# Performance work log

Hardware: AMD Instinct MI355X
Metric: run time of the kernel (lower is better)

Reference implementation:

```python
import jax, jax.numpy as jnp
import numpy as np

N = 50000          # nodes
E = 1_600_000      # edges (avg degree 32)
G = 512            # graphs in batch
IN_DIM = 128
HID = 64


def setup_inputs() -> dict:
    key = jax.random.key(0)
    ks = jax.random.split(key, 9)
    x = jax.random.normal(ks[0], (N, IN_DIM), dtype=jnp.float32)
    edge_index = jax.random.randint(ks[1], (2, E), 0, N, dtype=jnp.int64)
    edge_attr = jax.random.uniform(ks[2], (E,), dtype=jnp.float32)
    batch = jnp.sort(jax.random.randint(ks[3], (N,), 0, G, dtype=jnp.int64))
    W1 = jax.random.normal(ks[4], (IN_DIM, HID), dtype=jnp.float32) / np.sqrt(IN_DIM)
    b1 = jnp.zeros((HID,), dtype=jnp.float32)
    W2 = jax.random.normal(ks[5], (HID, HID), dtype=jnp.float32) / np.sqrt(HID)
    b2 = jnp.zeros((HID,), dtype=jnp.float32)
    Wlin = jax.random.normal(ks[6], (HID, 1), dtype=jnp.float32) / np.sqrt(HID)
    blin = jnp.zeros((1,), dtype=jnp.float32)
    return {"x": x, "edge_index": edge_index, "edge_attr": edge_attr,
            "batch": batch, "W1": W1, "b1": b1, "W2": W2, "b2": b2,
            "Wlin": Wlin, "blin": blin}


def reference(x, edge_index, edge_attr, batch, W1, b1, W2, b2, Wlin, blin):
    n = x.shape[0]
    src, dst = edge_index[0], edge_index[1]
    # GCNConv: add self-loops with weight 1, symmetric normalization
    loop = jnp.arange(n)
    src_f = jnp.concatenate([src, loop])
    dst_f = jnp.concatenate([dst, loop])
    w = jnp.concatenate([edge_attr, jnp.ones((n,), x.dtype)])
    deg = jax.ops.segment_sum(w, dst_f, num_segments=n)
    dis = jnp.where(deg > 0, jax.lax.rsqrt(jnp.maximum(deg, 1e-12)), 0.0)
    norm = dis[src_f] * w * dis[dst_f]  # [E+N]

    def conv(h, W, b):
        hw = h @ W                          # [N, HID]
        msg = norm[:, None] * hw[src_f]     # [E+N, HID]
        return jax.ops.segment_sum(msg, dst_f, num_segments=n) + b

    h = jax.nn.relu(conv(x, W1, b1))
    h = conv(h, W2, b2)
    # global_mean_pool over graph ids
    counts = jax.ops.segment_sum(jnp.ones((n,), h.dtype), batch, num_segments=G)
    pooled = jax.ops.segment_sum(h, batch, num_segments=G) / jnp.maximum(counts, 1.0)[:, None]
    return pooled @ Wlin + blin  # [G, 1]
```

## Files before the change

### kernel.cpp

```cpp
#include <hip/hip_runtime.h>

#define NN 50000
#define NE 1600000
#define NG 512
#define IN_DIM 128
#define HID 64

#define NB 128
#define NBK ((NN + NB - 1) / NB)
#define EBLK 512
#define EPB (NE / EBLK)

typedef unsigned short ushort_t;
typedef unsigned int uint_t;

static __device__ __forceinline__ ushort_t f2bf(float f) {
    uint_t u = __float_as_uint(f);
    u += 0x7FFFu + ((u >> 16) & 1u);
    return (ushort_t)(u >> 16);
}
static __device__ __forceinline__ float bflo(uint_t u) { return __uint_as_float(u << 16); }
static __device__ __forceinline__ float bfhi(uint_t u) { return __uint_as_float(u & 0xFFFF0000u); }

__global__ void cnt_kernel(const int* __restrict__ ei, int* __restrict__ pcnt) {
    __shared__ int h[NBK];
    for (int i = threadIdx.x; i < NBK; i += blockDim.x) h[i] = 0;
    __syncthreads();
    int base = blockIdx.x * EPB;
    for (int e = base + threadIdx.x; e < base + EPB; e += blockDim.x)
        atomicAdd(&h[ei[NE + e] >> 7], 1);
    __syncthreads();
    for (int i = threadIdx.x; i < NBK; i += blockDim.x)
        pcnt[(size_t)i * EBLK + blockIdx.x] = h[i];
}

__global__ void bscan_kernel(int* __restrict__ pcnt, int* __restrict__ tot) {
    __shared__ int s[EBLK];
    int k = blockIdx.x, t = threadIdx.x;
    int v = pcnt[(size_t)k * EBLK + t];
    s[t] = v;
    __syncthreads();
    for (int off = 1; off < EBLK; off <<= 1) {
        int add = (t >= off) ? s[t - off] : 0;
        __syncthreads();
        s[t] += add;
        __syncthreads();
    }
    pcnt[(size_t)k * EBLK + t] = s[t] - v;
    if (t == EBLK - 1) tot[k] = s[t];
}

__global__ void tscan_kernel(const int* __restrict__ tot, int* __restrict__ bbase) {
    __shared__ int s[512];
    int t = threadIdx.x;
    int v = (t < NBK) ? tot[t] : 0;
    s[t] = v;
    __syncthreads();
    for (int off = 1; off < 512; off <<= 1) {
        int add = (t >= off) ? s[t - off] : 0;
        __syncthreads();
        s[t] += add;
        __syncthreads();
    }
    if (t < NBK) bbase[t] = s[t] - v;
    if (t == NBK - 1) bbase[NBK] = s[t];
}

__global__ void scatter_kernel(const int* __restrict__ ei, const float* __restrict__ ea,
                               const int* __restrict__ pcnt, const int* __restrict__ bbase,
                               int2* __restrict__ recs) {
    __shared__ int curs[NBK];
    int b = blockIdx.x;
    for (int i = threadIdx.x; i < NBK; i += blockDim.x)
        curs[i] = bbase[i] + pcnt[(size_t)i * EBLK + b];
    __syncthreads();
    int base = b * EPB;
    for (int e = base + threadIdx.x; e < base + EPB; e += blockDim.x) {
        int dst = ei[NE + e];
        int src = ei[e];
        int k = dst >> 7;
        int pos = atomicAdd(&curs[k], 1);
        recs[pos] = make_int2(((dst & 127) << 17) | src, __float_as_int(ea[e]));
    }
}

__global__ void binfo2_kernel(const int2* __restrict__ recs, const int* __restrict__ bbase,
                              int* __restrict__ indeg, float* __restrict__ dis,
                              int* __restrict__ offs, int2* __restrict__ csr) {
    __shared__ float deg[NB];
    __shared__ int cnt[NB];
    __shared__ int sc[NB];
    __shared__ int curs[NB];
    __shared__ float wdst[NB];
    int k = blockIdx.x;
    int lo = k * NB;
    int nLoc = min(NB, NN - lo);
    int tid = threadIdx.x;
    for (int i = tid; i < nLoc; i += blockDim.x) { deg[i] = 0.f; cnt[i] = 0; }
    __syncthreads();
    int start = bbase[k], end = bbase[k + 1];
    for (int e = start + tid; e < end; e += blockDim.x) {
        int2 r = recs[e];
        int dl = r.x >> 17;
        atomicAdd(&deg[dl], __int_as_float(r.y));
        atomicAdd(&cnt[dl], 1);
    }
    __syncthreads();
    for (int i = tid; i < nLoc; i += blockDim.x) {
        float d = rsqrtf(deg[i] + 1.0f);
        wdst[i] = d;
        dis[lo + i] = d;
        indeg[lo + i] = cnt[i];
    }
    if (tid < NB) sc[tid] = (tid < nLoc) ? cnt[tid] : 0;
    __syncthreads();
    for (int off = 1; off < NB; off <<= 1) {
        int add = (tid < NB && tid >= off) ? sc[tid - off] : 0;
        __syncthreads();
        if (tid < NB) sc[tid] += add;
        __syncthreads();
    }
    if (tid < nLoc) {
        int ex = start + sc[tid] - cnt[tid];
        offs[lo + tid] = ex;
        curs[tid] = ex;
    }
    __syncthreads();
    for (int e = start + tid; e < end; e += blockDim.x) {
        int2 r = recs[e];
        int src = r.x & 0x1FFFF;
        int dl = r.x >> 17;
        float pw = __int_as_float(r.y) * wdst[dl];
        int pos = atomicAdd(&curs[dl], 1);
        csr[pos] = make_int2(src, __float_as_int(pw));
    }
}

template <int K>
__global__ __launch_bounds__(256) void gemm_kernel(const float* __restrict__ X,
                                                   const float* __restrict__ W,
                                                   const float* __restrict__ dis,
                                                   ushort_t* __restrict__ Yb) {
    __shared__ float w_lds[K * HID];
    __shared__ float x_lds[K][65];
    int tid = threadIdx.x;
    int rowbase = blockIdx.x * 64;
    for (int i = tid; i < K * HID; i += 256) w_lds[i] = W[i];
    for (int i = tid; i < 16 * K; i += 256) {
        int row = i / (K / 4);
        int k4 = i % (K / 4);
        int r = rowbase + row;
        float4 v = (r < NN) ? ((const float4*)(X + (size_t)r * K))[k4]
                            : make_float4(0.f, 0.f, 0.f, 0.f);
        x_lds[k4 * 4 + 0][row] = v.x;
        x_lds[k4 * 4 + 1][row] = v.y;
        x_lds[k4 * 4 + 2][row] = v.z;
        x_lds[k4 * 4 + 3][row] = v.w;
    }
    __syncthreads();
    int c0 = (tid & 15) * 4;
    int r0 = (tid >> 4) * 4;
    float acc[4][4] = {};
#pragma unroll 4
    for (int k = 0; k < K; ++k) {
        float x0 = x_lds[k][r0 + 0];
        float x1 = x_lds[k][r0 + 1];
        float x2 = x_lds[k][r0 + 2];
        float x3 = x_lds[k][r0 + 3];
        float4 wv = *(const float4*)&w_lds[k * HID + c0];
        acc[0][0] += x0 * wv.x; acc[0][1] += x0 * wv.y; acc[0][2] += x0 * wv.z; acc[0][3] += x0 * wv.w;
        acc[1][0] += x1 * wv.x; acc[1][1] += x1 * wv.y; acc[1][2] += x1 * wv.z; acc[1][3] += x1 * wv.w;
        acc[2][0] += x2 * wv.x; acc[2][1] += x2 * wv.y; acc[2][2] += x2 * wv.z; acc[2][3] += x2 * wv.w;
        acc[3][0] += x3 * wv.x; acc[3][1] += x3 * wv.y; acc[3][2] += x3 * wv.z; acc[3][3] += x3 * wv.w;
    }
#pragma unroll
    for (int i = 0; i < 4; ++i) {
        int r = rowbase + r0 + i;
        if (r < NN) {
            float dr = dis[r];
            ushort4 o;
            o.x = f2bf(dr * acc[i][0]); o.y = f2bf(dr * acc[i][1]);
            o.z = f2bf(dr * acc[i][2]); o.w = f2bf(dr * acc[i][3]);
            *(ushort4*)&Yb[(size_t)r * HID + c0] = o;
        }
    }
}

__global__ void gather1_kernel(const int2* __restrict__ csr,
                               const int* __restrict__ offs,
                               const int* __restrict__ indeg,
                               const float* __restrict__ dis,
                               const ushort_t* __restrict__ A1,
                               const float* __restrict__ b1,
                               float* __restrict__ OUT) {
    int node = blockIdx.x * 4 + (threadIdx.x >> 6);
    int lane = threadIdx.x & 63;
    if (node >= NN) return;
    int o  = lane >> 3;
    int cl = lane & 7;
    int start = offs[node];
    int n = indeg[node];
    float a0 = 0.f, a1 = 0.f, a2 = 0.f, a3 = 0.f;
    float a4 = 0.f, a5 = 0.f, a6 = 0.f, a7 = 0.f;
    for (int c = 0; c < n; c += 64) {
        int idx = c + lane;
        int2 rec = (idx < n) ? csr[start + idx] : make_int2(0, 0);
        int tmax = min(n - c, 64);
#pragma unroll 2
        for (int t = 0; t * 8 < tmax; ++t) {
            int sl = t * 8 + o;
            int key = __shfl(rec.x, sl, 64);
            float w = __int_as_float(__shfl(rec.y, sl, 64));
            uint4 v = *(const uint4*)(A1 + ((size_t)key << 6) + (cl << 3));
            a0 += w * bflo(v.x); a1 += w * bfhi(v.x);
            a2 += w * bflo(v.y); a3 += w * bfhi(v.y);
            a4 += w * bflo(v.z); a5 += w * bfhi(v.z);
            a6 += w * bflo(v.w); a7 += w * bfhi(v.w);
        }
    }
    a0 += __shfl_xor(a0, 8, 64); a0 += __shfl_xor(a0, 16, 64); a0 += __shfl_xor(a0, 32, 64);
    a1 += __shfl_xor(a1, 8, 64); a1 += __shfl_xor(a1, 16, 64); a1 += __shfl_xor(a1, 32, 64);
    a2 += __shfl_xor(a2, 8, 64); a2 += __shfl_xor(a2, 16, 64); a2 += __shfl_xor(a2, 32, 64);
    a3 += __shfl_xor(a3, 8, 64); a3 += __shfl_xor(a3, 16, 64); a3 += __shfl_xor(a3, 32, 64);
    a4 += __shfl_xor(a4, 8, 64); a4 += __shfl_xor(a4, 16, 64); a4 += __shfl_xor(a4, 32, 64);
    a5 += __shfl_xor(a5, 8, 64); a5 += __shfl_xor(a5, 16, 64); a5 += __shfl_xor(a5, 32, 64);
    a6 += __shfl_xor(a6, 8, 64); a6 += __shfl_xor(a6, 16, 64); a6 += __shfl_xor(a6, 32, 64);
    a7 += __shfl_xor(a7, 8, 64); a7 += __shfl_xor(a7, 16, 64); a7 += __shfl_xor(a7, 32, 64);
    if (o == 0) {
        float d = dis[node];
        uint4 sv = *(const uint4*)(A1 + ((size_t)node << 6) + (cl << 3));
        const float4* bv = (const float4*)(b1 + (cl << 3));
        float4 bA = bv[0], bB = bv[1];
        float o0 = fmaxf(a0 + d * bflo(sv.x) + bA.x, 0.f);
        float o1 = fmaxf(a1 + d * bfhi(sv.x) + bA.y, 0.f);
        float o2 = fmaxf(a2 + d * bflo(sv.y) + bA.z, 0.f);
        float o3 = fmaxf(a3 + d * bfhi(sv.y) + bA.w, 0.f);
        float o4 = fmaxf(a4 + d * bflo(sv.z) + bB.x, 0.f);
        float o5 = fmaxf(a5 + d * bfhi(sv.z) + bB.y, 0.f);
        float o6 = fmaxf(a6 + d * bflo(sv.w) + bB.z, 0.f);
        float o7 = fmaxf(a7 + d * bfhi(sv.w) + bB.w, 0.f);
        float* op = &OUT[((size_t)node << 6) + (cl << 3)];
        *(float4*)op       = make_float4(o0, o1, o2, o3);
        *(float4*)(op + 4) = make_float4(o4, o5, o6, o7);
    }
}

__global__ void gather2_kernel(const int2* __restrict__ csr,
                               const int* __restrict__ offs,
                               const int* __restrict__ indeg,
                               const float* __restrict__ dis,
                               const ushort_t* __restrict__ A2,
                               const float* __restrict__ b2,
                               const float* __restrict__ Wlin,
                               float* __restrict__ nodeval) {
    int node = blockIdx.x * 4 + (threadIdx.x >> 6);
    int lane = threadIdx.x & 63;
    if (node >= NN) return;
    int o  = lane >> 3;
    int cl = lane & 7;
    int start = offs[node];
    int n = indeg[node];
    float a0 = 0.f, a1 = 0.f, a2 = 0.f, a3 = 0.f;
    float a4 = 0.f, a5 = 0.f, a6 = 0.f, a7 = 0.f;
    for (int c = 0; c < n; c += 64) {
        int idx = c + lane;
        int2 rec = (idx < n) ? csr[start + idx] : make_int2(0, 0);
        int tmax = min(n - c, 64);
#pragma unroll 2
        for (int t = 0; t * 8 < tmax; ++t) {
            int sl = t * 8 + o;
            int key = __shfl(rec.x, sl, 64);
            float w = __int_as_float(__shfl(rec.y, sl, 64));
            uint4 v = *(const uint4*)(A2 + ((size_t)key << 6) + (cl << 3));
            a0 += w * bflo(v.x); a1 += w * bfhi(v.x);
            a2 += w * bflo(v.y); a3 += w * bfhi(v.y);
            a4 += w * bflo(v.z); a5 += w * bfhi(v.z);
            a6 += w * bflo(v.w); a7 += w * bfhi(v.w);
        }
    }
    a0 += __shfl_xor(a0, 8, 64); a0 += __shfl_xor(a0, 16, 64); a0 += __shfl_xor(a0, 32, 64);
    a1 += __shfl_xor(a1, 8, 64); a1 += __shfl_xor(a1, 16, 64); a1 += __shfl_xor(a1, 32, 64);
    a2 += __shfl_xor(a2, 8, 64); a2 += __shfl_xor(a2, 16, 64); a2 += __shfl_xor(a2, 32, 64);
    a3 += __shfl_xor(a3, 8, 64); a3 += __shfl_xor(a3, 16, 64); a3 += __shfl_xor(a3, 32, 64);
    a4 += __shfl_xor(a4, 8, 64); a4 += __shfl_xor(a4, 16, 64); a4 += __shfl_xor(a4, 32, 64);
    a5 += __shfl_xor(a5, 8, 64); a5 += __shfl_xor(a5, 16, 64); a5 += __shfl_xor(a5, 32, 64);
    a6 += __shfl_xor(a6, 8, 64); a6 += __shfl_xor(a6, 16, 64); a6 += __shfl_xor(a6, 32, 64);
    a7 += __shfl_xor(a7, 8, 64); a7 += __shfl_xor(a7, 16, 64); a7 += __shfl_xor(a7, 32, 64);
    float d = dis[node];
    uint4 sv = *(const uint4*)(A2 + ((size_t)node << 6) + (cl << 3));
    const float4* bv = (const float4*)(b2 + (cl << 3));
    float4 bA = bv[0], bB = bv[1];
    const float4* wv = (const float4*)(Wlin + (cl << 3));
    float4 wA = wv[0], wB = wv[1];
    float dot = (a0 + d * bflo(sv.x) + bA.x) * wA.x
              + (a1 + d * bfhi(sv.x) + bA.y) * wA.y
              + (a2 + d * bflo(sv.y) + bA.z) * wA.z
              + (a3 + d * bfhi(sv.y) + bA.w) * wA.w
              + (a4 + d * bflo(sv.z) + bB.x) * wB.x
              + (a5 + d * bfhi(sv.z) + bB.y) * wB.y
              + (a6 + d * bflo(sv.w) + bB.z) * wB.z
              + (a7 + d * bfhi(sv.w) + bB.w) * wB.w;
    dot += __shfl_xor(dot, 1, 64);
    dot += __shfl_xor(dot, 2, 64);
    dot += __shfl_xor(dot, 4, 64);
    if (lane == 0) nodeval[node] = dot;
}

__global__ void pool_final_kernel(const float* __restrict__ nodeval,
                                  const int* __restrict__ batch,
                                  const float* __restrict__ blin,
                                  float* __restrict__ out) {
    __shared__ int bnd[2];
    __shared__ float red[4];
    int g = blockIdx.x;
    if (threadIdx.x < 2) {
        int target = g + threadIdx.x;
        int lo = 0, hi = NN;
        while (lo < hi) {
            int mid = (lo + hi) >> 1;
            if (batch[mid] < target) lo = mid + 1; else hi = mid;
        }
        bnd[threadIdx.x] = lo;
    }
    __syncthreads();
    int s = bnd[0], e = bnd[1];
    float a = 0.f;
    for (int i = s + threadIdx.x; i < e; i += 256) a += nodeval[i];
    for (int off = 32; off > 0; off >>= 1) a += __shfl_down(a, off, 64);
    int lane = threadIdx.x & 63;
    int wv = threadIdx.x >> 6;
    if (lane == 0) red[wv] = a;
    __syncthreads();
    if (threadIdx.x == 0) {
        float t = red[0] + red[1] + red[2] + red[3];
        out[g] = t / fmaxf((float)(e - s), 1.0f) + blin[0];
    }
}

extern "C" void kernel_launch(void* const* d_in, const int* in_sizes, int n_in,
                              void* d_out, int out_size, void* d_ws, size_t ws_size,
                              hipStream_t stream) {
    const float* x     = (const float*)d_in[0];
    const int*   ei    = (const int*)d_in[1];
    const float* ea    = (const float*)d_in[2];
    const int*   batch = (const int*)d_in[3];
    const float* W1    = (const float*)d_in[4];
    const float* b1    = (const float*)d_in[5];
    const float* W2    = (const float*)d_in[6];
    const float* b2    = (const float*)d_in[7];
    const float* Wlin  = (const float*)d_in[8];
    const float* blin  = (const float*)d_in[9];
    float*       out   = (float*)d_out;

    char* ws = (char*)d_ws;
    auto alloc = [&](size_t bytes) {
        void* p = (void*)ws;
        ws += (bytes + 255) / 256 * 256;
        return p;
    };
    float*    dis     = (float*)alloc((size_t)NN * 4);
    int*      indeg   = (int*)alloc((size_t)NN * 4);
    int*      offs    = (int*)alloc((size_t)NN * 4);
    int*      pcnt    = (int*)alloc((size_t)NBK * EBLK * 4);
    int*      tot     = (int*)alloc((size_t)NBK * 4);
    int*      bbase   = (int*)alloc((size_t)(NBK + 1) * 4);
    int2*     recs    = (int2*)alloc((size_t)NE * 8);
    int2*     csr     = (int2*)alloc((size_t)NE * 8);
    float*    B       = (float*)alloc((size_t)NN * HID * 4);
    float*    nodeval = (float*)alloc((size_t)NN * 4);
    ushort_t* A1      = (ushort_t*)recs;
    ushort_t* A2      = (ushort_t*)recs + (size_t)NN * HID;

    cnt_kernel<<<EBLK, 256, 0, stream>>>(ei, pcnt);
    bscan_kernel<<<NBK, EBLK, 0, stream>>>(pcnt, tot);
    tscan_kernel<<<1, 512, 0, stream>>>(tot, bbase);
    scatter_kernel<<<EBLK, 256, 0, stream>>>(ei, ea, pcnt, bbase, recs);
    binfo2_kernel<<<NBK, 256, 0, stream>>>(recs, bbase, indeg, dis, offs, csr);

    gemm_kernel<IN_DIM><<<(NN + 63) / 64, 256, 0, stream>>>(x, W1, dis, A1);
    gather1_kernel<<<(NN + 3) / 4, 256, 0, stream>>>(csr, offs, indeg, dis, A1, b1, B);

    gemm_kernel<HID><<<(NN + 63) / 64, 256, 0, stream>>>(B, W2, dis, A2);
    gather2_kernel<<<(NN + 3) / 4, 256, 0, stream>>>(csr, offs, indeg, dis, A2, b2,
                                                     Wlin, nodeval);

    pool_final_kernel<<<NG, 256, 0, stream>>>(nodeval, batch, blin, out);
}
```

Before: 162.4 us.

## Fuse graph CSR build kernels into one cooperative kernel with grid syncs

```diff
diff --git a/kernel.cpp b/kernel.cpp
--- a/kernel.cpp
+++ b/kernel.cpp
@@ -1,4 +1,7 @@
 #include <hip/hip_runtime.h>
+#include <hip/hip_cooperative_groups.h>
+
+namespace cg = cooperative_groups;
 
 #define NN 50000
 #define NE 1600000
@@ -22,117 +25,130 @@
 static __device__ __forceinline__ float bflo(uint_t u) { return __uint_as_float(u << 16); }
 static __device__ __forceinline__ float bfhi(uint_t u) { return __uint_as_float(u & 0xFFFF0000u); }
 
-__global__ void cnt_kernel(const int* __restrict__ ei, int* __restrict__ pcnt) {
+__global__ void build_kernel(const int* __restrict__ ei, const float* __restrict__ ea,
+                             int* __restrict__ pcnt, int* __restrict__ tot,
+                             int* __restrict__ bbase, int* __restrict__ indeg,
+                             float* __restrict__ dis, int* __restrict__ offs,
+                             int2* __restrict__ recs, int2* __restrict__ csr) {
+    cg::grid_group grid = cg::this_grid();
+    int b = blockIdx.x;
+    int tid = threadIdx.x;
+
     __shared__ int h[NBK];
-    for (int i = threadIdx.x; i < NBK; i += blockDim.x) h[i] = 0;
-    __syncthreads();
-    int base = blockIdx.x * EPB;
-    for (int e = base + threadIdx.x; e < base + EPB; e += blockDim.x)
-        atomicAdd(&h[ei[NE + e] >> 7], 1);
-    __syncthreads();
-    for (int i = threadIdx.x; i < NBK; i += blockDim.x)
-        pcnt[(size_t)i * EBLK + blockIdx.x] = h[i];
-}
-
-__global__ void bscan_kernel(int* __restrict__ pcnt, int* __restrict__ tot) {
-    __shared__ int s[EBLK];
-    int k = blockIdx.x, t = threadIdx.x;
-    int v = pcnt[(size_t)k * EBLK + t];
-    s[t] = v;
-    __syncthreads();
-    for (int off = 1; off < EBLK; off <<= 1) {
-        int add = (t >= off) ? s[t - off] : 0;
-        __syncthreads();
-        s[t] += add;
-        __syncthreads();
-    }
-    pcnt[(size_t)k * EBLK + t] = s[t] - v;
-    if (t == EBLK - 1) tot[k] = s[t];
-}
-
-__global__ void tscan_kernel(const int* __restrict__ tot, int* __restrict__ bbase) {
-    __shared__ int s[512];
-    int t = threadIdx.x;
-    int v = (t < NBK) ? tot[t] : 0;
-    s[t] = v;
-    __syncthreads();
-    for (int off = 1; off < 512; off <<= 1) {
-        int add = (t >= off) ? s[t - off] : 0;
-        __syncthreads();
-        s[t] += add;
-        __syncthreads();
-    }
-    if (t < NBK) bbase[t] = s[t] - v;
-    if (t == NBK - 1) bbase[NBK] = s[t];
-}
-
-__global__ void scatter_kernel(const int* __restrict__ ei, const float* __restrict__ ea,
-                               const int* __restrict__ pcnt, const int* __restrict__ bbase,
-                               int2* __restrict__ recs) {
-    __shared__ int curs[NBK];
-    int b = blockIdx.x;
-    for (int i = threadIdx.x; i < NBK; i += blockDim.x)
-        curs[i] = bbase[i] + pcnt[(size_t)i * EBLK + b];
-    __syncthreads();
-    int base = b * EPB;
-    for (int e = base + threadIdx.x; e < base + EPB; e += blockDim.x) {
-        int dst = ei[NE + e];
-        int src = ei[e];
-        int k = dst >> 7;
-        int pos = atomicAdd(&curs[k], 1);
-        recs[pos] = make_int2(((dst & 127) << 17) | src, __float_as_int(ea[e]));
-    }
-}
-
-__global__ void binfo2_kernel(const int2* __restrict__ recs, const int* __restrict__ bbase,
-                              int* __restrict__ indeg, float* __restrict__ dis,
-                              int* __restrict__ offs, int2* __restrict__ csr) {
-    __shared__ float deg[NB];
-    __shared__ int cnt[NB];
+    __shared__ int s[256];
+    __shared__ float degs[NB];
+    __shared__ int cnts[NB];
     __shared__ int sc[NB];
     __shared__ int curs[NB];
     __shared__ float wdst[NB];
-    int k = blockIdx.x;
-    int lo = k * NB;
-    int nLoc = min(NB, NN - lo);
-    int tid = threadIdx.x;
-    for (int i = tid; i < nLoc; i += blockDim.x) { deg[i] = 0.f; cnt[i] = 0; }
-    __syncthreads();
-    int start = bbase[k], end = bbase[k + 1];
-    for (int e = start + tid; e < end; e += blockDim.x) {
-        int2 r = recs[e];
-        int dl = r.x >> 17;
-        atomicAdd(&deg[dl], __int_as_float(r.y));
-        atomicAdd(&cnt[dl], 1);
-    }
-    __syncthreads();
-    for (int i = tid; i < nLoc; i += blockDim.x) {
-        float d = rsqrtf(deg[i] + 1.0f);
-        wdst[i] = d;
-        dis[lo + i] = d;
-        indeg[lo + i] = cnt[i];
-    }
-    if (tid < NB) sc[tid] = (tid < nLoc) ? cnt[tid] : 0;
-    __syncthreads();
-    for (int off = 1; off < NB; off <<= 1) {
-        int add = (tid < NB && tid >= off) ? sc[tid - off] : 0;
-        __syncthreads();
-        if (tid < NB) sc[tid] += add;
-        __syncthreads();
-    }
-    if (tid < nLoc) {
-        int ex = start + sc[tid] - cnt[tid];
-        offs[lo + tid] = ex;
-        curs[tid] = ex;
-    }
-    __syncthreads();
-    for (int e = start + tid; e < end; e += blockDim.x) {
-        int2 r = recs[e];
-        int src = r.x & 0x1FFFF;
-        int dl = r.x >> 17;
-        float pw = __int_as_float(r.y) * wdst[dl];
-        int pos = atomicAdd(&curs[dl], 1);
-        csr[pos] = make_int2(src, __float_as_int(pw));
+
+    for (int i = tid; i < NBK; i += 256) h[i] = 0;
+    __syncthreads();
+    {
+        int base = b * EPB;
+        for (int e = base + tid; e < base + EPB; e += 256)
+            atomicAdd(&h[ei[NE + e] >> 7], 1);
+    }
+    __syncthreads();
+    for (int i = tid; i < NBK; i += 256)
+        pcnt[(size_t)i * EBLK + b] = h[i];
+    grid.sync();
+
+    if (b < NBK) {
+        size_t base = (size_t)b * EBLK;
+        int v0 = pcnt[base + 2 * tid];
+        int v1 = pcnt[base + 2 * tid + 1];
+        int pairsum = v0 + v1;
+        s[tid] = pairsum;
+        __syncthreads();
+        for (int off = 1; off < 256; off <<= 1) {
+            int add = (tid >= off) ? s[tid - off] : 0;
+            __syncthreads();
+            s[tid] += add;
+            __syncthreads();
+        }
+        int exc = s[tid] - pairsum;
+        pcnt[base + 2 * tid]     = exc;
+        pcnt[base + 2 * tid + 1] = exc + v0;
+        if (tid == 255) tot[b] = s[255];
+    }
+    grid.sync();
+
+    if (b == 0) {
+        int i0 = 2 * tid, i1 = 2 * tid + 1;
+        int v0 = (i0 < NBK) ? tot[i0] : 0;
+        int v1 = (i1 < NBK) ? tot[i1] : 0;
+        int pairsum = v0 + v1;
+        s[tid] = pairsum;
+        __syncthreads();
+        for (int off = 1; off < 256; off <<= 1) {
+            int add = (tid >= off) ? s[tid - off] : 0;
+            __syncthreads();
+            s[tid] += add;
+            __syncthreads();
+        }
+        int exc = s[tid] - pairsum;
+        if (i0 <= NBK) bbase[i0] = exc;
+        if (i1 <= NBK) bbase[i1] = exc + v0;
+    }
+    grid.sync();
+
+    for (int i = tid; i < NBK; i += 256)
+        h[i] = bbase[i] + pcnt[(size_t)i * EBLK + b];
+    __syncthreads();
+    {
+        int base = b * EPB;
+        for (int e = base + tid; e < base + EPB; e += 256) {
+            int dst = ei[NE + e];
+            int src = ei[e];
+            int k = dst >> 7;
+            int pos = atomicAdd(&h[k], 1);
+            recs[pos] = make_int2(((dst & 127) << 17) | src, __float_as_int(ea[e]));
+        }
+    }
+    grid.sync();
+
+    if (b < NBK) {
+        int lo = b * NB;
+        int nLoc = min(NB, NN - lo);
+        for (int i = tid; i < nLoc; i += 256) { degs[i] = 0.f; cnts[i] = 0; }
+        __syncthreads();
+        int start = bbase[b], end = bbase[b + 1];
+        for (int e = start + tid; e < end; e += 256) {
+            int2 r = recs[e];
+            int dl = r.x >> 17;
+            atomicAdd(&degs[dl], __int_as_float(r.y));
+            atomicAdd(&cnts[dl], 1);
+        }
+        __syncthreads();
+        for (int i = tid; i < nLoc; i += 256) {
+            float d = rsqrtf(degs[i] + 1.0f);
+            wdst[i] = d;
+            dis[lo + i] = d;
+            indeg[lo + i] = cnts[i];
+        }
+        if (tid < NB) sc[tid] = (tid < nLoc) ? cnts[tid] : 0;
+        __syncthreads();
+        for (int off = 1; off < NB; off <<= 1) {
+            int add = (tid < NB && tid >= off) ? sc[tid - off] : 0;
+            __syncthreads();
+            if (tid < NB) sc[tid] += add;
+            __syncthreads();
+        }
+        if (tid < nLoc) {
+            int ex = start + sc[tid] - cnts[tid];
+            offs[lo + tid] = ex;
+            curs[tid] = ex;
+        }
+        __syncthreads();
+        for (int e = start + tid; e < end; e += 256) {
+            int2 r = recs[e];
+            int src = r.x & 0x1FFFF;
+            int dl = r.x >> 17;
+            float pw = __int_as_float(r.y) * wdst[dl];
+            int pos = atomicAdd(&curs[dl], 1);
+            csr[pos] = make_int2(src, __float_as_int(pw));
+        }
     }
 }
 
@@ -371,11 +387,13 @@
     ushort_t* A1      = (ushort_t*)recs;
     ushort_t* A2      = (ushort_t*)recs + (size_t)NN * HID;
 
-    cnt_kernel<<<EBLK, 256, 0, stream>>>(ei, pcnt);
-    bscan_kernel<<<NBK, EBLK, 0, stream>>>(pcnt, tot);
-    tscan_kernel<<<1, 512, 0, stream>>>(tot, bbase);
-    scatter_kernel<<<EBLK, 256, 0, stream>>>(ei, ea, pcnt, bbase, recs);
-    binfo2_kernel<<<NBK, 256, 0, stream>>>(recs, bbase, indeg, dis, offs, csr);
+    {
+        void* args[] = {(void*)&ei, (void*)&ea, (void*)&pcnt, (void*)&tot,
+                        (void*)&bbase, (void*)&indeg, (void*)&dis, (void*)&offs,
+                        (void*)&recs, (void*)&csr};
+        hipLaunchCooperativeKernel((void*)build_kernel, dim3(EBLK), dim3(256),
+                                   args, 0, stream);
+    }
 
     gemm_kernel<IN_DIM><<<(NN + 63) / 64, 256, 0, stream>>>(x, W1, dis, A1);
     gather1_kernel<<<(NN + 3) / 4, 256, 0, stream>>>(csr, offs, indeg, dis, A1, b1, B);
```

After: 400.8 us. 2.47x slower.
